# Kernel tuning notes

Measured on AMD Instinct MI355X. Metric: run time of the kernel, lower is better.

The kernel has to match this reference:

```python
import jax, jax.numpy as jnp
import numpy as np

B, T, C, H = 2, 2048, 1024, 16


def setup_inputs() -> dict:
    key = jax.random.key(0)
    ks = jax.random.split(key, 9)
    s = 1.0 / np.sqrt(C)
    return {
        "query": jax.random.normal(ks[0], (B, T, C), dtype=jnp.float32),
        "Wq": jax.random.normal(ks[1], (C, C), dtype=jnp.float32) * s,
        "bq": jnp.zeros((C,), dtype=jnp.float32),
        "Wk": jax.random.normal(ks[2], (C, C), dtype=jnp.float32) * s,
        "bk": jnp.zeros((C,), dtype=jnp.float32),
        "Wv": jax.random.normal(ks[3], (C, C), dtype=jnp.float32) * s,
        "bv": jnp.zeros((C,), dtype=jnp.float32),
        "Wp": jax.random.normal(ks[4], (C, C), dtype=jnp.float32) * s,
        "bp": jnp.zeros((C,), dtype=jnp.float32),
        "n_head": H,
    }


def reference(query, Wq, bq, Wk, bk, Wv, bv, Wp, bp, n_head):
    b, t, c = query.shape
    d = c // n_head
    # QKV projections -> [b, h, t, d]
    q = (query @ Wq + bq).reshape(b, t, n_head, d).transpose(0, 2, 1, 3)
    k = (query @ Wk + bk).reshape(b, t, n_head, d).transpose(0, 2, 1, 3)
    v = (query @ Wv + bv).reshape(b, t, n_head, d).transpose(0, 2, 1, 3)
    scale = 1.0 / jnp.sqrt(jnp.asarray(d, dtype=query.dtype))
    att = jnp.einsum('bhtd,bhsd->bhts', q, k) * scale  # [b,h,t,t]
    causal = jnp.tril(jnp.ones((t, t), dtype=bool))
    att = jnp.where(causal[None, None, :, :], att, -jnp.inf)
    att = jax.nn.softmax(att, axis=-1)
    y = jnp.einsum('bhts,bhsd->bhtd', att, v)  # [b,h,t,d]
    y = y.transpose(0, 2, 1, 3).reshape(b, t, c)
    return y @ Wp + bp
```

## Files before the change

### kernel.cpp

```cpp
#include <hip/hip_runtime.h>
#include <math.h>

#define B_ 2
#define T_ 2048
#define C_ 1024
#define H_ 16
#define D_ 64
#define M_ (B_*T_)

typedef __bf16 bf16x8 __attribute__((ext_vector_type(8)));
typedef __bf16 bf16x4 __attribute__((ext_vector_type(4)));
typedef float  f32x4  __attribute__((ext_vector_type(4)));

__device__ __forceinline__ unsigned short f2bf(float f) {
    unsigned int u = __float_as_uint(f);
    u += 0x7FFFu + ((u >> 16) & 1u);
    return (unsigned short)(u >> 16);
}

__device__ __forceinline__ void gload16(const void* g, void* l) {
    __builtin_amdgcn_global_load_lds(
        (const __attribute__((address_space(1))) void*)g,
        (__attribute__((address_space(3))) void*)l, 16, 0, 0);
}

__global__ __launch_bounds__(256) void prep_kernel(
    const float* __restrict__ X, unsigned short* __restrict__ Xb,
    const float* __restrict__ W0, const float* __restrict__ W1,
    const float* __restrict__ W2, const float* __restrict__ W3,
    unsigned short* __restrict__ T0, unsigned short* __restrict__ T1,
    unsigned short* __restrict__ T2, unsigned short* __restrict__ T3)
{
    const int tid = threadIdx.x;
    if (blockIdx.x < 2048) {
        const size_t i = ((size_t)blockIdx.x * 256 + tid) * 8;
        const float4 a = *(const float4*)&X[i];
        const float4 b = *(const float4*)&X[i + 4];
        ushort4 s0, s1;
        s0.x = f2bf(a.x); s0.y = f2bf(a.y); s0.z = f2bf(a.z); s0.w = f2bf(a.w);
        s1.x = f2bf(b.x); s1.y = f2bf(b.y); s1.z = f2bf(b.z); s1.w = f2bf(b.w);
        *(ushort4*)&Xb[i]     = s0;
        *(ushort4*)&Xb[i + 4] = s1;
        return;
    }
    const int bz = blockIdx.x - 2048;
    const int z = bz >> 10, rem = bz & 1023;
    const float* W; unsigned short* Wt;
    switch (z) {
        case 0: W = W0; Wt = T0; break;
        case 1: W = W1; Wt = T1; break;
        case 2: W = W2; Wt = T2; break;
        default: W = W3; Wt = T3; break;
    }
    __shared__ unsigned short tile[32][33];
    const int k0 = (rem >> 5) * 32, n0 = (rem & 31) * 32;
    {
        const int r = tid >> 3, c = (tid & 7) * 4;
        const float4 v = *(const float4*)&W[(size_t)(k0 + r)*C_ + n0 + c];
        tile[c+0][r] = f2bf(v.x);
        tile[c+1][r] = f2bf(v.y);
        tile[c+2][r] = f2bf(v.z);
        tile[c+3][r] = f2bf(v.w);
    }
    __syncthreads();
    {
        const int r = tid >> 3, c = (tid & 7) * 4;
        ushort4 s;
        s.x = tile[r][c+0]; s.y = tile[r][c+1]; s.z = tile[r][c+2]; s.w = tile[r][c+3];
        *(ushort4*)&Wt[(size_t)(n0 + r)*C_ + k0 + c] = s;
    }
}

__global__ __launch_bounds__(256) void gemm_mfma_kernel(
    const unsigned short* __restrict__ A, const unsigned short* __restrict__ Bt,
    const float* __restrict__ b0, const float* __restrict__ b1,
    const float* __restrict__ b2,
    void* __restrict__ out0, void* __restrict__ out1, void* __restrict__ out2,
    int mode)
{
    __shared__ __align__(16) unsigned short Als[2][128 * 32];
    __shared__ __align__(16) unsigned short Bls[2][128 * 32];

    const int tid  = threadIdx.x;
    const int lane = tid & 63;
    const int wave = tid >> 6;
    const int wm = wave >> 1, wn = wave & 1;
    const int l15 = lane & 15, quad = lane >> 4;
    const int m0 = blockIdx.y * 128, n0 = blockIdx.x * 128;
    const int srow = lane >> 2;
    const int scol = (lane & 3) * 8;

    const f32x4 zero4 = {0.f, 0.f, 0.f, 0.f};
    f32x4 acc[4][4];
    #pragma unroll
    for (int i = 0; i < 4; ++i)
        #pragma unroll
        for (int j = 0; j < 4; ++j) acc[i][j] = zero4;

    for (int k0 = 0; k0 < C_; k0 += 64) {
        __syncthreads();
        #pragma unroll
        for (int h = 0; h < 2; ++h) {
            #pragma unroll
            for (int u = 0; u < 2; ++u) {
                const int r = wave*32 + u*16 + srow;
                gload16(&A [(size_t)(m0 + r)*C_ + k0 + h*32 + scol],
                        &Als[h][(wave*32 + u*16)*32]);
                gload16(&Bt[(size_t)(n0 + r)*C_ + k0 + h*32 + scol],
                        &Bls[h][(wave*32 + u*16)*32]);
            }
        }
        __syncthreads();

        #pragma unroll
        for (int h = 0; h < 2; ++h) {
            bf16x8 af[4], bfr[4];
            #pragma unroll
            for (int i = 0; i < 4; ++i)
                af[i] = *(const bf16x8*)&Als[h][(wm*64 + i*16 + l15)*32 + quad*8];
            #pragma unroll
            for (int j = 0; j < 4; ++j)
                bfr[j] = *(const bf16x8*)&Bls[h][(wn*64 + j*16 + l15)*32 + quad*8];

            #pragma unroll
            for (int i = 0; i < 4; ++i)
                #pragma unroll
                for (int j = 0; j < 4; ++j)
                    acc[i][j] = __builtin_amdgcn_mfma_f32_16x16x32_bf16(
                        af[i], bfr[j], acc[i][j], 0, 0, 0);
        }
    }

    if (mode == 0) {
        float* o0 = (float*)out0;
        #pragma unroll
        for (int j = 0; j < 4; ++j) {
            const int n = n0 + wn*64 + j*16 + l15;
            const float bias = b0[n];
            #pragma unroll
            for (int i = 0; i < 4; ++i)
                #pragma unroll
                for (int r = 0; r < 4; ++r) {
                    const int m = m0 + wm*64 + i*16 + quad*4 + r;
                    o0[(size_t)m*C_ + n] = acc[i][j][r] + bias;
                }
        }
        return;
    }
}

__global__ __launch_bounds__(512, 2) void gemm256_qkv_kernel(
    const unsigned short* __restrict__ A, const unsigned short* __restrict__ Bt,
    const float* __restrict__ b0, const float* __restrict__ b1,
    const float* __restrict__ b2,
    unsigned short* __restrict__ outq, unsigned short* __restrict__ outk,
    unsigned short* __restrict__ outv)
{
    __shared__ __align__(16) unsigned short lds[4 * 16384];

    const int tid  = threadIdx.x;
    const int lane = tid & 63;
    const int wave = tid >> 6;
    const int l15  = lane & 15, quad = lane >> 4;
    const int wm   = wave >> 2, wn = wave & 3;
    const int m0   = blockIdx.y * 256, n0 = blockIdx.x * 256;

    const int lrow = lane >> 2;
    const int csw  = ((lane & 3) ^ ((lane >> 3) & 3)) * 8;
    const int sw8  = (quad ^ ((l15 >> 1) & 3)) * 8;

#define STAGE(tt) do {                                                         \
        const int bi_ = ((tt) & 3) << 14;                                      \
        const int k0_ = (tt) << 5;                                             \
        const int ra_ = m0 + wave*32 + lrow;                                   \
        const int rb_ = n0 + wave*32 + lrow;                                   \
        gload16(&A [(size_t)ra_*C_ + k0_ + csw],      &lds[bi_ + wave*1024]);  \
        gload16(&Bt[(size_t)rb_*C_ + k0_ + csw],      &lds[bi_ + 8192 + wave*1024]); \
        gload16(&A [(size_t)(ra_+16)*C_ + k0_ + csw], &lds[bi_ + wave*1024 + 512]);  \
        gload16(&Bt[(size_t)(rb_+16)*C_ + k0_ + csw], &lds[bi_ + 8192 + wave*1024 + 512]); \
    } while (0)

    const f32x4 zero4 = {0.f, 0.f, 0.f, 0.f};
    f32x4 acc[8][4];
    #pragma unroll
    for (int i = 0; i < 8; ++i)
        #pragma unroll
        for (int j = 0; j < 4; ++j) acc[i][j] = zero4;

    STAGE(0); STAGE(1); STAGE(2);

    for (int t = 0; t < 32; ++t) {
        const int bi = (t & 3) << 14;
        __builtin_amdgcn_s_barrier();
        __builtin_amdgcn_sched_barrier(0);
        if (t < 29) {
            STAGE(t + 3);
            asm volatile("s_waitcnt vmcnt(12)" ::: "memory");
        } else if (t == 29) {
            asm volatile("s_waitcnt vmcnt(8)" ::: "memory");
        } else if (t == 30) {
            asm volatile("s_waitcnt vmcnt(4)" ::: "memory");
        } else {
            asm volatile("s_waitcnt vmcnt(0)" ::: "memory");
        }
        __builtin_amdgcn_s_barrier();
        __builtin_amdgcn_sched_barrier(0);

        const unsigned short* Ab = &lds[bi];
        const unsigned short* Bb = &lds[bi + 8192];

        bf16x8 bfr[4], af[4];
        #pragma unroll
        for (int j = 0; j < 4; ++j)
            bfr[j] = *(const bf16x8*)&Bb[(wn*64 + j*16 + l15)*32 + sw8];
        #pragma unroll
        for (int i = 0; i < 4; ++i)
            af[i] = *(const bf16x8*)&Ab[(wm*128 + i*16 + l15)*32 + sw8];

        __builtin_amdgcn_s_setprio(1);
        #pragma unroll
        for (int i = 0; i < 4; ++i)
            #pragma unroll
            for (int j = 0; j < 4; ++j)
                acc[i][j] = __builtin_amdgcn_mfma_f32_16x16x32_bf16(
                    af[i], bfr[j], acc[i][j], 0, 0, 0);
        __builtin_amdgcn_s_setprio(0);

        #pragma unroll
        for (int i = 0; i < 4; ++i)
            af[i] = *(const bf16x8*)&Ab[(wm*128 + 64 + i*16 + l15)*32 + sw8];

        __builtin_amdgcn_s_setprio(1);
        #pragma unroll
        for (int i = 0; i < 4; ++i)
            #pragma unroll
            for (int j = 0; j < 4; ++j)
                acc[4+i][j] = __builtin_amdgcn_mfma_f32_16x16x32_bf16(
                    af[i], bfr[j], acc[4+i][j], 0, 0, 0);
        __builtin_amdgcn_s_setprio(0);
    }
#undef STAGE

    __syncthreads();

    unsigned short* Ep = &lds[wave * 8192];
    const int which = n0 >> 10;
    const int c0 = (n0 & 1023) + wn * 64;
    const int h  = c0 >> 6;
    const int bb = m0 >> 11;
    const int t0 = (m0 & (T_ - 1)) + wm * 128;
    const int bh = bb * H_ + h;
    const float* bp = (which == 0) ? b0 : (which == 1 ? b1 : b2);
    const float qscale = (which == 0) ? 0.18033688f : 1.0f;

    if (which < 2) {
        __bf16* Eb = (__bf16*)Ep;
        #pragma unroll
        for (int j = 0; j < 4; ++j) {
            const int cl = j*16 + l15;
            const float bias = bp[c0 + cl];
            #pragma unroll
            for (int i = 0; i < 8; ++i)
                #pragma unroll
                for (int r = 0; r < 4; ++r)
                    Eb[(i*16 + quad*4 + r)*64 + cl] =
                        (__bf16)((acc[i][j][r] + bias) * qscale);
        }
        unsigned short* op = (which == 0) ? outq : outk;
        const int row8 = lane >> 3, chunk = lane & 7;
        #pragma unroll
        for (int u = 0; u < 16; ++u) {
            const int row = u*8 + row8;
            const uint4 v = *(const uint4*)&Ep[row*64 + chunk*8];
            *(uint4*)&op[((size_t)bh*T_ + t0 + row)*D_ + chunk*8] = v;
        }
    } else {
        #pragma unroll
        for (int j = 0; j < 4; ++j) {
            const int cl = j*16 + l15;
            const float bias = bp[c0 + cl];
            const int xo = (cl & 7) * 8;
            #pragma unroll
            for (int i = 0; i < 8; ++i) {
                bf16x4 pk = {(__bf16)(acc[i][j][0] + bias),
                             (__bf16)(acc[i][j][1] + bias),
                             (__bf16)(acc[i][j][2] + bias),
                             (__bf16)(acc[i][j][3] + bias)};
                *(bf16x4*)&Ep[cl*128 + ((i*16 + quad*4) ^ xo)] = pk;
            }
        }
        const int d4 = lane >> 4, chunk = lane & 15;
        #pragma unroll
        for (int u = 0; u < 16; ++u) {
            const int d = u*4 + d4;
            const uint4 v = *(const uint4*)&Ep[d*128 + ((chunk*8) ^ ((d & 7)*8))];
            *(uint4*)&outv[((size_t)bh*D_ + d)*T_ + t0 + chunk*8] = v;
        }
    }
}

__global__ __launch_bounds__(256) void flash_mfma_kernel(
    const unsigned short* __restrict__ Qs, const unsigned short* __restrict__ Ks,
    const unsigned short* __restrict__ Vts, unsigned short* __restrict__ Y,
    float* __restrict__ parts, float* __restrict__ lbase)
{
    __shared__ __align__(16) unsigned short Pls[4 * 2048];

    const int tid  = threadIdx.x;
    const int lane = tid & 63, wave = tid >> 6;
    const int l15  = lane & 15, quad = lane >> 4;
    const int job  = blockIdx.x >> 5;
    const int bh   = blockIdx.x & 31;
    const bool isA = (job < 8);
    const int a    = isA ? job : job - 8;

    int qts[2], slos[2], shis[2], slots[2], nseg;
    if (isA) {
        qts[0] = a;      slos[0] = 0;        shis[0] = 2*a + 2;  slots[0] = -1;
        qts[1] = 15 - a; slos[1] = 0;        shis[1] = 15 - 2*a; slots[1] = 0;
        nseg = 2;
    } else {
        qts[0] = 15 - a; slos[0] = 15 - 2*a; shis[0] = 32 - 2*a; slots[0] = 1;
        nseg = 1;
    }

    unsigned short* Pw = &Pls[wave * 2048];
    const int b_ = bh >> 4, h_ = bh & (H_ - 1);
    const f32x4 zero4 = {0.f, 0.f, 0.f, 0.f};

    const unsigned short* Kb = Ks  + ((size_t)bh*T_ + l15)*D_ + quad*8;
    const unsigned short* Vb = Vts + ((size_t)bh*D_ + l15)*T_ + quad*8;

    for (int sg = 0; sg < nseg; ++sg) {
        const int qt  = qts[sg];
        const int qw0 = qt * 128 + wave * 32;

        bf16x8 qf[2][2];
        #pragma unroll
        for (int i = 0; i < 2; ++i)
            #pragma unroll
            for (int kd = 0; kd < 2; ++kd)
                qf[i][kd] = *(const bf16x8*)&Qs[((size_t)bh*T_ + qw0 + i*16 + l15)*D_
                                                + kd*32 + quad*8];

        f32x4 o[2][4];
        #pragma unroll
        for (int i = 0; i < 2; ++i)
            #pragma unroll
            for (int jd = 0; jd < 4; ++jd) o[i][jd] = zero4;
        float lsum[2] = {0.f, 0.f};

        for (int it = slos[sg]; it < shis[sg]; ++it) {
            const int s0 = it * 64;
            if (s0 > qw0 + 31) continue;

            bf16x8 kf[2][4];
            const unsigned short* Kp = Kb + (size_t)s0 * D_;
            #pragma unroll
            for (int kd = 0; kd < 2; ++kd)
                #pragma unroll
                for (int j = 0; j < 4; ++j)
                    kf[kd][j] = *(const bf16x8*)&Kp[(j*16)*D_ + kd*32];

            bf16x8 vf[2][4];
            const unsigned short* Vp = Vb + s0;
            #pragma unroll
            for (int kk = 0; kk < 2; ++kk)
                #pragma unroll
                for (int jd = 0; jd < 4; ++jd)
                    vf[kk][jd] = *(const bf16x8*)&Vp[(jd*16)*T_ + kk*32];

            f32x4 st[2][4];
            #pragma unroll
            for (int i = 0; i < 2; ++i)
                #pragma unroll
                for (int j = 0; j < 4; ++j) st[i][j] = zero4;
            #pragma unroll
            for (int kd = 0; kd < 2; ++kd) {
                __builtin_amdgcn_s_setprio(1);
                #pragma unroll
                for (int i = 0; i < 2; ++i)
                    #pragma unroll
                    for (int j = 0; j < 4; ++j)
                        st[i][j] = __builtin_amdgcn_mfma_f32_16x16x32_bf16(
                            kf[kd][j], qf[i][kd], st[i][j], 0, 0, 0);
                __builtin_amdgcn_s_setprio(0);
            }

            const bool diag = (s0 + 63 > qw0);
            #pragma unroll
            for (int i = 0; i < 2; ++i) {
                const int qrow = qw0 + i*16 + l15;
                #pragma unroll
                for (int j = 0; j < 4; ++j)
                    #pragma unroll
                    for (int r = 0; r < 4; ++r) {
                        float e = exp2f(st[i][j][r]);
                        if (diag && (s0 + j*16 + quad*4 + r > qrow)) e = 0.f;
                        st[i][j][r] = e;
                        lsum[i] += e;
                    }
            }

            #pragma unroll
            for (int i = 0; i < 2; ++i)
                #pragma unroll
                for (int j = 0; j < 4; ++j) {
                    bf16x4 pk = {(__bf16)st[i][j][0], (__bf16)st[i][j][1],
                                 (__bf16)st[i][j][2], (__bf16)st[i][j][3]};
                    *(bf16x4*)&Pw[(((j>>1)*2 + i)*4 + (j&1)*2 + (quad>>1))*128
                                   + l15*8 + (quad&1)*4] = pk;
                }

            #pragma unroll
            for (int kk = 0; kk < 2; ++kk) {
                bf16x8 pf[2];
                #pragma unroll
                for (int i = 0; i < 2; ++i)
                    pf[i] = *(const bf16x8*)&Pw[(kk*2 + i)*512 + lane*8];
                __builtin_amdgcn_s_setprio(1);
                #pragma unroll
                for (int i = 0; i < 2; ++i)
                    #pragma unroll
                    for (int jd = 0; jd < 4; ++jd)
                        o[i][jd] = __builtin_amdgcn_mfma_f32_16x16x32_bf16(
                            vf[kk][jd], pf[i], o[i][jd], 0, 0, 0);
                __builtin_amdgcn_s_setprio(0);
            }
        }

        #pragma unroll
        for (int i = 0; i < 2; ++i) {
            float v = lsum[i];
            v += __shfl_xor(v, 16, 64);
            v += __shfl_xor(v, 32, 64);
            lsum[i] = v;
        }

        if (slots[sg] < 0) {
            #pragma unroll
            for (int i = 0; i < 2; ++i) {
                const float inv = 1.0f / lsum[i];
                const int t = qw0 + i*16 + l15;
                #pragma unroll
                for (int jd = 0; jd < 4; ++jd) {
                    bf16x4 pk = {(__bf16)(o[i][jd][0] * inv),
                                 (__bf16)(o[i][jd][1] * inv),
                                 (__bf16)(o[i][jd][2] * inv),
                                 (__bf16)(o[i][jd][3] * inv)};
                    *(bf16x4*)&Y[((size_t)(b_*T_ + t))*C_ + h_*D_ + jd*16 + quad*4]
                        = pk;
                }
            }
        } else {
            const int gpi = bh*16 + a*2 + slots[sg];
            float* Op = parts + (size_t)gpi*8192;
            float* Lp = lbase + gpi*128;
            #pragma unroll
            for (int i = 0; i < 2; ++i) {
                const int tl = wave*32 + i*16 + l15;
                if (quad == 0) Lp[tl] = lsum[i];
                #pragma unroll
                for (int jd = 0; jd < 4; ++jd)
                    *(f32x4*)&Op[(size_t)tl*64 + jd*16 + quad*4] = o[i][jd];
            }
        }
    }
}

__global__ __launch_bounds__(256) void merge_kernel(
    const float* __restrict__ parts, const float* __restrict__ lbase,
    unsigned short* __restrict__ Y)
{
    const int pair = blockIdx.x;
    const int bh = pair >> 3, p = pair & 7;
    const int qt = 15 - p;
    const int g0 = bh*16 + p*2;
    const float* O0 = parts + (size_t)g0*8192;
    const float* O1 = O0 + 8192;
    const float* L0 = lbase + g0*128;
    const float* L1 = L0 + 128;

    const int tid = threadIdx.x;
    const int r = tid >> 1, c0 = (tid & 1) * 32;
    const float inv = 1.0f / (L0[r] + L1[r]);
    const int b = bh >> 4, h = bh & (H_ - 1);
    const int t = qt*128 + r;
    #pragma unroll
    for (int k = 0; k < 8; ++k) {
        const f32x4 a  = *(const f32x4*)&O0[(size_t)r*64 + c0 + k*4];
        const f32x4 bb = *(const f32x4*)&O1[(size_t)r*64 + c0 + k*4];
        bf16x4 pk = {(__bf16)((a[0]+bb[0])*inv), (__bf16)((a[1]+bb[1])*inv),
                     (__bf16)((a[2]+bb[2])*inv), (__bf16)((a[3]+bb[3])*inv)};
        *(bf16x4*)&Y[((size_t)(b*T_ + t))*C_ + h*D_ + c0 + k*4] = pk;
    }
}

extern "C" void kernel_launch(void* const* d_in, const int* in_sizes, int n_in,
                              void* d_out, int out_size, void* d_ws, size_t ws_size,
                              hipStream_t stream) {
    const float* query = (const float*)d_in[0];
    const float* Wq = (const float*)d_in[1];
    const float* bq = (const float*)d_in[2];
    const float* Wk = (const float*)d_in[3];
    const float* bk = (const float*)d_in[4];
    const float* Wv = (const float*)d_in[5];
    const float* bv = (const float*)d_in[6];
    const float* Wp = (const float*)d_in[7];
    const float* bp = (const float*)d_in[8];
    float* out = (float*)d_out;

    char* ws = (char*)d_ws;
    unsigned short* qbf   = (unsigned short*)(ws);
    unsigned short* kbf   = (unsigned short*)(ws + 8388608);
    unsigned short* vtbf  = (unsigned short*)(ws + 16777216);
    unsigned short* WtP   = (unsigned short*)(ws + 25165824);
    unsigned short* WtQKV = (unsigned short*)(ws + 27262976);
    unsigned short* yb    = (unsigned short*)(ws + 33554432);
    unsigned short* qx    = (unsigned short*)(ws + 41943040);
    float* lbase = (float*)(ws + 27262976);
    float* parts = out;

    prep_kernel<<<6144, 256, 0, stream>>>(
        query, qx, Wq, Wk, Wv, Wp,
        WtQKV, WtQKV + (size_t)C_*C_, WtQKV + 2*(size_t)C_*C_, WtP);

    gemm256_qkv_kernel<<<dim3(12, 16), 512, 0, stream>>>(
        qx, WtQKV, bq, bk, bv, qbf, kbf, vtbf);

    flash_mfma_kernel<<<512, 256, 0, stream>>>(qbf, kbf, vtbf, yb, parts, lbase);
    merge_kernel<<<256, 256, 0, stream>>>(parts, lbase, yb);

    gemm_mfma_kernel<<<dim3(C_/128, M_/128), 256, 0, stream>>>(
        yb, WtP, bp, bp, bp, out, nullptr, nullptr, 0);
}
```

Before: 230.4 us.

## Stage K/V tiles through LDS in flash kernel and halve proj GEMM M-tile

Each flash-attention block now cooperatively loads the 64-key K and V^T tiles into shared memory with global_load_lds, so all four waves share them instead of each wave fetching its own copy from global memory. This adds two barriers per key iteration and removes the setprio hints around the MFMAs. Separately, the output projection GEMM is specialised and switched to a 64x128 tile, doubling the grid to 512 blocks for better CU occupancy, at the cost of less B-tile reuse.

New measurement: 204.1 us. -11.4%, faster.

```diff
diff --git a/kernel.cpp b/kernel.cpp
--- a/kernel.cpp
+++ b/kernel.cpp
@@ -71,14 +71,11 @@
     }
 }
 
-__global__ __launch_bounds__(256) void gemm_mfma_kernel(
+__global__ __launch_bounds__(256) void gemm_proj_kernel(
     const unsigned short* __restrict__ A, const unsigned short* __restrict__ Bt,
-    const float* __restrict__ b0, const float* __restrict__ b1,
-    const float* __restrict__ b2,
-    void* __restrict__ out0, void* __restrict__ out1, void* __restrict__ out2,
-    int mode)
+    const float* __restrict__ bias, float* __restrict__ out)
 {
-    __shared__ __align__(16) unsigned short Als[2][128 * 32];
+    __shared__ __align__(16) unsigned short Als[2][64 * 32];
     __shared__ __align__(16) unsigned short Bls[2][128 * 32];
 
     const int tid  = threadIdx.x;
@@ -86,14 +83,14 @@
     const int wave = tid >> 6;
     const int wm = wave >> 1, wn = wave & 1;
     const int l15 = lane & 15, quad = lane >> 4;
-    const int m0 = blockIdx.y * 128, n0 = blockIdx.x * 128;
+    const int m0 = blockIdx.y * 64, n0 = blockIdx.x * 128;
     const int srow = lane >> 2;
     const int scol = (lane & 3) * 8;
 
     const f32x4 zero4 = {0.f, 0.f, 0.f, 0.f};
-    f32x4 acc[4][4];
+    f32x4 acc[2][4];
     #pragma unroll
-    for (int i = 0; i < 4; ++i)
+    for (int i = 0; i < 2; ++i)
         #pragma unroll
         for (int j = 0; j < 4; ++j) acc[i][j] = zero4;
 
@@ -101,11 +98,11 @@
         __syncthreads();
         #pragma unroll
         for (int h = 0; h < 2; ++h) {
+            gload16(&A[(size_t)(m0 + wave*16 + srow)*C_ + k0 + h*32 + scol],
+                    &Als[h][(wave*16)*32]);
             #pragma unroll
             for (int u = 0; u < 2; ++u) {
                 const int r = wave*32 + u*16 + srow;
-                gload16(&A [(size_t)(m0 + r)*C_ + k0 + h*32 + scol],
-                        &Als[h][(wave*32 + u*16)*32]);
                 gload16(&Bt[(size_t)(n0 + r)*C_ + k0 + h*32 + scol],
                         &Bls[h][(wave*32 + u*16)*32]);
             }
@@ -114,16 +111,16 @@
 
         #pragma unroll
         for (int h = 0; h < 2; ++h) {
-            bf16x8 af[4], bfr[4];
-            #pragma unroll
-            for (int i = 0; i < 4; ++i)
-                af[i] = *(const bf16x8*)&Als[h][(wm*64 + i*16 + l15)*32 + quad*8];
+            bf16x8 af[2], bfr[4];
+            #pragma unroll
+            for (int i = 0; i < 2; ++i)
+                af[i] = *(const bf16x8*)&Als[h][(wm*32 + i*16 + l15)*32 + quad*8];
             #pragma unroll
             for (int j = 0; j < 4; ++j)
                 bfr[j] = *(const bf16x8*)&Bls[h][(wn*64 + j*16 + l15)*32 + quad*8];
 
             #pragma unroll
-            for (int i = 0; i < 4; ++i)
+            for (int i = 0; i < 2; ++i)
                 #pragma unroll
                 for (int j = 0; j < 4; ++j)
                     acc[i][j] = __builtin_amdgcn_mfma_f32_16x16x32_bf16(
@@ -131,21 +128,17 @@
         }
     }
 
-    if (mode == 0) {
-        float* o0 = (float*)out0;
-        #pragma unroll
-        for (int j = 0; j < 4; ++j) {
-            const int n = n0 + wn*64 + j*16 + l15;
-            const float bias = b0[n];
-            #pragma unroll
-            for (int i = 0; i < 4; ++i)
-                #pragma unroll
-                for (int r = 0; r < 4; ++r) {
-                    const int m = m0 + wm*64 + i*16 + quad*4 + r;
-                    o0[(size_t)m*C_ + n] = acc[i][j][r] + bias;
-                }
-        }
-        return;
+    #pragma unroll
+    for (int j = 0; j < 4; ++j) {
+        const int n = n0 + wn*64 + j*16 + l15;
+        const float bv = bias[n];
+        #pragma unroll
+        for (int i = 0; i < 2; ++i)
+            #pragma unroll
+            for (int r = 0; r < 4; ++r) {
+                const int m = m0 + wm*32 + i*16 + quad*4 + r;
+                out[(size_t)m*C_ + n] = acc[i][j][r] + bv;
+            }
     }
 }
 
@@ -304,6 +297,8 @@
     const unsigned short* __restrict__ Vts, unsigned short* __restrict__ Y,
     float* __restrict__ parts, float* __restrict__ lbase)
 {
+    __shared__ __align__(16) unsigned short Kls[64 * 64];
+    __shared__ __align__(16) unsigned short Vls[64 * 64];
     __shared__ __align__(16) unsigned short Pls[4 * 2048];
 
     const int tid  = threadIdx.x;
@@ -325,11 +320,10 @@
     }
 
     unsigned short* Pw = &Pls[wave * 2048];
+    const int kd_s = wave >> 1;
+    const int c8_s = (kd_s * 4 + quad) * 8;
     const int b_ = bh >> 4, h_ = bh & (H_ - 1);
     const f32x4 zero4 = {0.f, 0.f, 0.f, 0.f};
-
-    const unsigned short* Kb = Ks  + ((size_t)bh*T_ + l15)*D_ + quad*8;
-    const unsigned short* Vb = Vts + ((size_t)bh*D_ + l15)*T_ + quad*8;
 
     for (int sg = 0; sg < nseg; ++sg) {
         const int qt  = qts[sg];
@@ -352,39 +346,37 @@
 
         for (int it = slos[sg]; it < shis[sg]; ++it) {
             const int s0 = it * 64;
+            __syncthreads();
+            #pragma unroll
+            for (int u = 0; u < 2; ++u) {
+                const int cu  = 2*wave + u;
+                const int row = ((cu & 3) << 4) + l15;
+                gload16(&Ks [((size_t)bh*T_ + s0 + row)*D_ + c8_s],
+                        (char*)Kls + cu*1024);
+                gload16(&Vts[((size_t)bh*D_ + row)*T_ + s0 + c8_s],
+                        (char*)Vls + cu*1024);
+            }
+            __syncthreads();
+
             if (s0 > qw0 + 31) continue;
 
-            bf16x8 kf[2][4];
-            const unsigned short* Kp = Kb + (size_t)s0 * D_;
-            #pragma unroll
-            for (int kd = 0; kd < 2; ++kd)
+            f32x4 st[2][4];
+            #pragma unroll
+            for (int i = 0; i < 2; ++i)
+                #pragma unroll
+                for (int j = 0; j < 4; ++j) st[i][j] = zero4;
+            #pragma unroll
+            for (int kd = 0; kd < 2; ++kd) {
+                bf16x8 kf[4];
                 #pragma unroll
                 for (int j = 0; j < 4; ++j)
-                    kf[kd][j] = *(const bf16x8*)&Kp[(j*16)*D_ + kd*32];
-
-            bf16x8 vf[2][4];
-            const unsigned short* Vp = Vb + s0;
-            #pragma unroll
-            for (int kk = 0; kk < 2; ++kk)
-                #pragma unroll
-                for (int jd = 0; jd < 4; ++jd)
-                    vf[kk][jd] = *(const bf16x8*)&Vp[(jd*16)*T_ + kk*32];
-
-            f32x4 st[2][4];
-            #pragma unroll
-            for (int i = 0; i < 2; ++i)
-                #pragma unroll
-                for (int j = 0; j < 4; ++j) st[i][j] = zero4;
-            #pragma unroll
-            for (int kd = 0; kd < 2; ++kd) {
-                __builtin_amdgcn_s_setprio(1);
+                    kf[j] = *(const bf16x8*)&Kls[lane*8 + j*512 + kd*2048];
                 #pragma unroll
                 for (int i = 0; i < 2; ++i)
                     #pragma unroll
                     for (int j = 0; j < 4; ++j)
                         st[i][j] = __builtin_amdgcn_mfma_f32_16x16x32_bf16(
-                            kf[kd][j], qf[i][kd], st[i][j], 0, 0, 0);
-                __builtin_amdgcn_s_setprio(0);
+                            kf[j], qf[i][kd], st[i][j], 0, 0, 0);
             }
 
             const bool diag = (s0 + 63 > qw0);
@@ -414,18 +406,19 @@
 
             #pragma unroll
             for (int kk = 0; kk < 2; ++kk) {
-                bf16x8 pf[2];
+                bf16x8 pf[2], vf[4];
                 #pragma unroll
                 for (int i = 0; i < 2; ++i)
                     pf[i] = *(const bf16x8*)&Pw[(kk*2 + i)*512 + lane*8];
-                __builtin_amdgcn_s_setprio(1);
+                #pragma unroll
+                for (int jd = 0; jd < 4; ++jd)
+                    vf[jd] = *(const bf16x8*)&Vls[lane*8 + jd*512 + kk*2048];
                 #pragma unroll
                 for (int i = 0; i < 2; ++i)
                     #pragma unroll
                     for (int jd = 0; jd < 4; ++jd)
                         o[i][jd] = __builtin_amdgcn_mfma_f32_16x16x32_bf16(
-                            vf[kk][jd], pf[i], o[i][jd], 0, 0, 0);
-                __builtin_amdgcn_s_setprio(0);
+                            vf[jd], pf[i], o[i][jd], 0, 0, 0);
             }
         }
 
@@ -531,6 +524,6 @@
     flash_mfma_kernel<<<512, 256, 0, stream>>>(qbf, kbf, vtbf, yb, parts, lbase);
     merge_kernel<<<256, 256, 0, stream>>>(parts, lbase, yb);
 
-    gemm_mfma_kernel<<<dim3(C_/128, M_/128), 256, 0, stream>>>(
-        yb, WtP, bp, bp, bp, out, nullptr, nullptr, 0);
-}
+    gemm_proj_kernel<<<dim3(C_/128, M_/64), 256, 0, stream>>>(
+        yb, WtP, bp, out);
+}
```
